# Kernel tuning notes

Hardware: AMD Instinct MI355X
Metric: run time of the kernel (lower is better)

The kernel has to match this reference:

```python
import jax, jax.numpy as jnp
import numpy as np

B, C, CI, T, H, W = 4, 256, 128, 8, 28, 28
EPS = 1e-5


def setup_inputs() -> dict:
    key = jax.random.key(0)
    ks = jax.random.split(key, 12)
    s = 0.02
    return {
        "x": jax.random.normal(ks[0], (B, C, T, H, W), jnp.float32),
        "Wg": jax.random.normal(ks[1], (CI, C), jnp.float32) * s,
        "bg": jax.random.normal(ks[2], (CI,), jnp.float32) * s,
        "Wt": jax.random.normal(ks[3], (CI, C), jnp.float32) * s,
        "bt": jax.random.normal(ks[4], (CI,), jnp.float32) * s,
        "Wp": jax.random.normal(ks[5], (CI, C), jnp.float32) * s,
        "bp": jax.random.normal(ks[6], (CI,), jnp.float32) * s,
        "Ww": jax.random.normal(ks[7], (C, CI), jnp.float32) * s,
        "bw": jax.random.normal(ks[8], (C,), jnp.float32) * s,
        "gamma": jax.random.normal(ks[9], (C,), jnp.float32) * s + 1.0,
        "beta": jax.random.normal(ks[10], (C,), jnp.float32) * s,
        "rmean": jax.random.normal(ks[11], (C,), jnp.float32) * s,
        "rvar": jax.random.uniform(jax.random.fold_in(key, 99), (C,), jnp.float32, 0.5, 1.5),
    }


def reference(x, Wg, bg, Wt, bt, Wp, bp, Ww, bw, gamma, beta, rmean, rvar):
    b, c, t, h, w = x.shape
    n = t * h * w
    xf = x.reshape(b, c, n)                                   # [B,C,N]
    # 1x1x1 conv projections == per-position linear maps
    g = jnp.einsum('oc,bcn->bno', Wg, xf) + bg                # [B,N,Ci]
    th = jnp.einsum('oc,bcn->bno', Wt, xf) + bt               # [B,N,Ci]
    ph = jnp.einsum('oc,bcn->bon', Wp, xf) + bp[None, :, None]  # [B,Ci,N]
    f = jnp.einsum('bnc,bcm->bnm', th, ph)                    # [B,N,N] attention logits
    attn = jax.nn.softmax(f, axis=-1)
    y = jnp.einsum('bnm,bmo->bno', attn, g)                   # [B,N,Ci]
    wy = jnp.einsum('co,bno->bcn', Ww, y) + bw[None, :, None]  # [B,C,N]
    # BatchNorm3d (eval mode: running stats)
    inv = gamma / jnp.sqrt(rvar + EPS)
    wy = wy * inv[None, :, None] + (beta - rmean * inv)[None, :, None]
    z = wy + xf                                               # residual
    return z.reshape(b, c, t, h, w)
```

## Files before the change

kernel.cpp:

```cpp
#include <hip/hip_runtime.h>
#include <hip/hip_bf16.h>
#include <hip/hip_fp8.h>

#define BB 4
#define CC 256
#define CI 128
#define NN 6272
#define LOG2E 1.4426950408889634f

#define KSTRIDE 136
#define VSTRIDE 72
#define KBUF (64 * KSTRIDE)
#define VBUF (128 * VSTRIDE)

typedef __attribute__((ext_vector_type(8))) __bf16 bf16x8;
typedef __attribute__((ext_vector_type(4))) __bf16 bf16x4;
typedef __attribute__((ext_vector_type(4))) float f32x4;
typedef __attribute__((ext_vector_type(16))) float f32x16;

__device__ __forceinline__ unsigned cvtpk_fp8(float a, float b) {
  unsigned r;
  asm("v_cvt_pk_fp8_f32 %0, %1, %2" : "=v"(r) : "v"(a), "v"(b));
  return r;
}

__device__ __forceinline__ unsigned char to_fp8(float v) {
  __hip_fp8_e4m3 t(v);
  return *reinterpret_cast<unsigned char*>(&t);
}

__global__ void nlb_prep(const float* __restrict__ Wg, const float* __restrict__ bg,
                         const float* __restrict__ Wt, const float* __restrict__ bt,
                         const float* __restrict__ Wp, const float* __restrict__ bp,
                         const float* __restrict__ Ww, const float* __restrict__ bw,
                         const float* __restrict__ gamma, const float* __restrict__ beta,
                         const float* __restrict__ rmean, const float* __restrict__ rvar,
                         __bf16* __restrict__ wall, float* __restrict__ ball,
                         __bf16* __restrict__ wwb, float* __restrict__ scale,
                         float* __restrict__ shift) {
  int idx = blockIdx.x * 256 + threadIdx.x;
  if (idx < 384 * 256) {
    int o = idx >> 8, c = idx & 255;
    float v, bv;
    if (o < 128)      { v = Wt[o * 256 + c] * LOG2E;  bv = bt[o] * LOG2E; }
    else if (o < 256) { v = Wp[(o - 128) * 256 + c]; bv = bp[o - 128]; }
    else              { v = Wg[(o - 256) * 256 + c]; bv = bg[o - 256]; }
    wall[idx] = (__bf16)v;
    if (c == 0) ball[o] = bv;
  } else if (idx < 384 * 256 + 256 * 128) {
    int i = idx - 384 * 256;
    wwb[i] = (__bf16)Ww[i];
  } else if (idx < 384 * 256 + 256 * 128 + 256) {
    int c = idx - (384 * 256 + 256 * 128);
    float inv = gamma[c] * rsqrtf(rvar[c] + 1e-5f);
    scale[c] = inv;
    shift[c] = (bw[c] - rmean[c]) * inv + beta[c];
  }
}

__launch_bounds__(256)
__global__ void nlb_proj(const float* __restrict__ x, const __bf16* __restrict__ wall,
                         const float* __restrict__ ball,
                         unsigned char* __restrict__ Q8, unsigned char* __restrict__ K8,
                         unsigned char* __restrict__ V8t) {
  const int nb = blockIdx.x;
  const int b  = blockIdx.y;
  const int tid = threadIdx.x;
  const int lane = tid & 63, w = tid >> 6;
  const int n0 = nb * 64;
  const int r = lane & 15, g = lane >> 4;

  __shared__ __bf16 xl[64][40];

  const float* xb = x + (size_t)b * CC * NN;
  f32x4 acc[6][4] = {};

  const int snn = tid & 63;
  const int skg = tid >> 6;

  for (int k0 = 0; k0 < 256; k0 += 32) {
    bf16x8 tmp;
#pragma unroll
    for (int i = 0; i < 8; ++i)
      tmp[i] = (__bf16)xb[(size_t)(k0 + skg * 8 + i) * NN + n0 + snn];
    __syncthreads();
    *reinterpret_cast<bf16x8*>(&xl[snn][skg * 8]) = tmp;
    __syncthreads();

    bf16x8 bfrag[4];
#pragma unroll
    for (int j = 0; j < 4; ++j)
      bfrag[j] = *reinterpret_cast<const bf16x8*>(&xl[j * 16 + r][g * 8]);
#pragma unroll
    for (int mb = 0; mb < 6; ++mb) {
      bf16x8 afrag = *reinterpret_cast<const bf16x8*>(
          &wall[(size_t)(mb * 64 + w * 16 + r) * 256 + k0 + g * 8]);
#pragma unroll
      for (int j = 0; j < 4; ++j)
        acc[mb][j] = __builtin_amdgcn_mfma_f32_16x16x32_bf16(afrag, bfrag[j], acc[mb][j], 0, 0, 0);
    }
  }

#pragma unroll
  for (int mb = 0; mb < 6; ++mb) {
    const int m0 = mb * 64 + w * 16;
    if (m0 < 256) {
      unsigned char* dst = (m0 < 128) ? Q8 : K8;
      const int obase = (m0 < 128) ? m0 : (m0 - 128);
#pragma unroll
      for (int j = 0; j < 4; ++j) {
        int n = n0 + j * 16 + r;
        union { unsigned char bch[4]; unsigned u; } pk;
#pragma unroll
        for (int reg = 0; reg < 4; ++reg) {
          int o = m0 + g * 4 + reg;
          pk.bch[reg] = to_fp8(acc[mb][j][reg] + ball[o]);
        }
        *reinterpret_cast<unsigned*>(&dst[((size_t)b * NN + n) * CI + obase + g * 4]) = pk.u;
      }
    } else {
#pragma unroll
      for (int j = 0; j < 4; ++j) {
        int n = n0 + j * 16 + r;
#pragma unroll
        for (int reg = 0; reg < 4; ++reg) {
          int o = m0 + g * 4 + reg;
          float v = acc[mb][j][reg] + ball[o];
          V8t[((size_t)b * CI + (o - 256)) * NN + n] = to_fp8(v);
        }
      }
    }
  }
}

__launch_bounds__(256, 2)
__global__ void nlb_attn(const unsigned char* __restrict__ Q8,
                         const unsigned char* __restrict__ K8,
                         const unsigned char* __restrict__ V8t,
                         __bf16* __restrict__ Y) {
  const int bid = blockIdx.x;
  const int swz = (bid & 7) * 49 + (bid >> 3);
  const int b  = swz / 98;
  const int qb = swz % 98;
  const int tid = threadIdx.x, lane = tid & 63, w = tid >> 6;
  const int c = lane & 31, hi = lane >> 5;
  const int wq = w & 1, h = w >> 1;
  const int q0 = qb * 64 + wq * 32;

  const unsigned char* Qb = Q8  + (size_t)b * NN * CI;
  const char* Kb = (const char*)(K8 + (size_t)b * NN * CI);
  const char* Vb = (const char*)(V8t + (size_t)b * CI * NN);

  __shared__ __align__(16) char sm[2 * KBUF + 2 * VBUF];
  __shared__ float mls[2][64];

  uint4 gk0, gk1, gv0, gv1;
  const char* ksrc = Kb + tid * 32;
  const char* vsrc = Vb + (size_t)(tid >> 1) * NN + (tid & 1) * 32;
  auto gload = [&]() {
    gk0 = *reinterpret_cast<const uint4*>(ksrc);
    gk1 = *reinterpret_cast<const uint4*>(ksrc + 16);
    gv0 = *reinterpret_cast<const uint4*>(vsrc);
    gv1 = *reinterpret_cast<const uint4*>(vsrc + 16);
    ksrc += 8192; vsrc += 64;
  };
  char* const kd_base = sm + (tid >> 2) * KSTRIDE + (tid & 3) * 32;
  char* const vd_base = sm + 2 * KBUF + (tid >> 1) * VSTRIDE + (tid & 1) * 32;
  auto swrite = [&](int bb) {
    char* kd = kd_base + bb * KBUF;
    *reinterpret_cast<uint2*>(kd + 0)  = make_uint2(gk0.x, gk0.y);
    *reinterpret_cast<uint2*>(kd + 8)  = make_uint2(gk0.z, gk0.w);
    *reinterpret_cast<uint2*>(kd + 16) = make_uint2(gk1.x, gk1.y);
    *reinterpret_cast<uint2*>(kd + 24) = make_uint2(gk1.z, gk1.w);
    char* vd = vd_base + bb * VBUF;
    *reinterpret_cast<uint2*>(vd + 0)  = make_uint2(gv0.x, gv0.y);
    *reinterpret_cast<uint2*>(vd + 8)  = make_uint2(gv0.z, gv0.w);
    *reinterpret_cast<uint2*>(vd + 16) = make_uint2(gv1.x, gv1.y);
    *reinterpret_cast<uint2*>(vd + 24) = make_uint2(gv1.z, gv1.w);
  };

  long qf[8];
#pragma unroll
  for (int kc = 0; kc < 8; ++kc)
    qf[kc] = *reinterpret_cast<const long*>(&Qb[(size_t)(q0 + c) * CI + kc * 16 + hi * 8]);

  f32x16 yacc[4] = {};
  float l_acc = 0.f;

  gload();
  swrite(0);
  __syncthreads();

  int buf = 0;
  for (int t = 0; t < 98; ++t) {
    if (t + 1 < 98) gload();
    const char* kl = sm + buf * KBUF;
    const char* vl = sm + 2 * KBUF + buf * VBUF;

    f32x16 s;
#pragma unroll
    for (int i = 0; i < 16; ++i) s[i] = -4.f;
    __builtin_amdgcn_s_setprio(1);
#pragma unroll
    for (int kc = 0; kc < 8; ++kc) {
      long kf = *reinterpret_cast<const long*>(
          kl + (h * 32 + c) * KSTRIDE + kc * 16 + hi * 8);
      s = __builtin_amdgcn_mfma_f32_32x32x16_fp8_fp8(kf, qf[kc], s, 0, 0, 0);
    }
    __builtin_amdgcn_s_setprio(0);

#pragma unroll
    for (int reg = 0; reg < 16; ++reg) s[reg] = exp2f(s[reg]);
    float l0 = ((s[0] + s[1]) + (s[2] + s[3])) + ((s[4] + s[5]) + (s[6] + s[7]));
    float l1 = ((s[8] + s[9]) + (s[10] + s[11])) + ((s[12] + s[13]) + (s[14] + s[15]));
    l_acc += l0 + l1;

    unsigned pw[4];
#pragma unroll
    for (int i = 0; i < 4; ++i) {
      unsigned lo  = cvtpk_fp8(s[4 * i + 0], s[4 * i + 1]);
      unsigned hi2 = cvtpk_fp8(s[4 * i + 2], s[4 * i + 3]);
      pw[i] = __builtin_amdgcn_perm(hi2, lo, 0x05040100);
    }

    __builtin_amdgcn_s_setprio(1);
#pragma unroll
    for (int ch = 0; ch < 2; ++ch) {
      unsigned A = pw[ch * 2 + 0], B = pw[ch * 2 + 1];
      unsigned sX = (unsigned)__shfl_xor((int)(hi ? A : B), 32);
      unsigned plo = hi ? sX : A;
      unsigned phi = hi ? B : sX;
      long pa = (long)(((unsigned long long)phi << 32) | plo);
#pragma unroll
      for (int cb = 0; cb < 4; ++cb) {
        long vf = *reinterpret_cast<const long*>(
            vl + (cb * 32 + c) * VSTRIDE + h * 32 + ch * 16 + hi * 8);
        yacc[cb] = __builtin_amdgcn_mfma_f32_32x32x16_fp8_fp8(pa, vf, yacc[cb], 0, 0, 0);
      }
    }
    __builtin_amdgcn_s_setprio(0);

    if (t + 1 < 98) swrite(buf ^ 1);
    __syncthreads();
    buf ^= 1;
  }

  float l_full = l_acc + __shfl_xor(l_acc, 32);

  float* scr = (float*)sm;
  if (h == 1) {
    float* base = scr + wq * 4096;
#pragma unroll
    for (int cb = 0; cb < 4; ++cb)
#pragma unroll
      for (int reg = 0; reg < 16; ++reg)
        base[(cb * 16 + reg) * 64 + lane] = yacc[cb][reg];
    mls[wq][lane] = l_full;
  }
  __syncthreads();
  if (h == 0) {
    const float* base = scr + wq * 4096;
    float il = 1.f / (l_full + mls[wq][lane]);
    float ilq[16];
#pragma unroll
    for (int reg = 0; reg < 16; ++reg) {
      int qloc = (reg & 3) + 8 * (reg >> 2) + 4 * hi;
      ilq[reg] = __shfl(il, qloc);
    }
#pragma unroll
    for (int cb = 0; cb < 4; ++cb) {
#pragma unroll
      for (int reg = 0; reg < 16; ++reg) {
        int qloc = (reg & 3) + 8 * (reg >> 2) + 4 * hi;
        float v = (yacc[cb][reg] + base[(cb * 16 + reg) * 64 + lane]) * ilq[reg];
        Y[((size_t)b * NN + q0 + qloc) * CI + cb * 32 + c] = (__bf16)v;
      }
    }
  }
}

__launch_bounds__(256)
__global__ void nlb_out(const __bf16* __restrict__ Y, const __bf16* __restrict__ wwb,
                        const float* __restrict__ scale, const float* __restrict__ shift,
                        const float* __restrict__ x, float* __restrict__ out) {
  const int nb = blockIdx.x;
  const int mb = blockIdx.y;
  const int b  = blockIdx.z;
  const int tid = threadIdx.x, lane = tid & 63, w = tid >> 6;
  const int r = lane & 15, g = lane >> 4;
  const int n0 = nb * 64, c0 = mb * 64 + w * 16;

  const __bf16* Yb = Y + (size_t)b * NN * CI;
  f32x4 acc[4] = {};
#pragma unroll
  for (int k0 = 0; k0 < 128; k0 += 32) {
    bf16x8 af = *reinterpret_cast<const bf16x8*>(&wwb[(size_t)(c0 + r) * CI + k0 + g * 8]);
#pragma unroll
    for (int j = 0; j < 4; ++j) {
      bf16x8 bfg = *reinterpret_cast<const bf16x8*>(
          &Yb[(size_t)(n0 + j * 16 + r) * CI + k0 + g * 8]);
      acc[j] = __builtin_amdgcn_mfma_f32_16x16x32_bf16(af, bfg, acc[j], 0, 0, 0);
    }
  }
  const float* xb = x + (size_t)b * CC * NN;
  float* ob = out + (size_t)b * CC * NN;
#pragma unroll
  for (int j = 0; j < 4; ++j) {
    int n = n0 + j * 16 + r;
#pragma unroll
    for (int reg = 0; reg < 4; ++reg) {
      int cc = c0 + g * 4 + reg;
      size_t off = (size_t)cc * NN + n;
      ob[off] = acc[j][reg] * scale[cc] + shift[cc] + xb[off];
    }
  }
}

extern "C" void kernel_launch(void* const* d_in, const int* in_sizes, int n_in,
                              void* d_out, int out_size, void* d_ws, size_t ws_size,
                              hipStream_t stream) {
  (void)in_sizes; (void)n_in; (void)out_size; (void)ws_size;
  const float* x     = (const float*)d_in[0];
  const float* Wg    = (const float*)d_in[1];
  const float* bg    = (const float*)d_in[2];
  const float* Wt    = (const float*)d_in[3];
  const float* bt    = (const float*)d_in[4];
  const float* Wp    = (const float*)d_in[5];
  const float* bp    = (const float*)d_in[6];
  const float* Ww    = (const float*)d_in[7];
  const float* bw    = (const float*)d_in[8];
  const float* gamma = (const float*)d_in[9];
  const float* beta  = (const float*)d_in[10];
  const float* rmean = (const float*)d_in[11];
  const float* rvar  = (const float*)d_in[12];
  float* out = (float*)d_out;

  char* ws = (char*)d_ws;
  __bf16* wall = (__bf16*)(ws + 0);
  float*  ball = (float*)(ws + 196608);
  __bf16* wwb  = (__bf16*)(ws + 198144);
  float*  scl  = (float*)(ws + 263680);
  float*  shf  = (float*)(ws + 264704);
  unsigned char* Q8 = (unsigned char*)(ws + 265728);
  unsigned char* K8 = (unsigned char*)(ws + 3476992);
  unsigned char* V8 = (unsigned char*)(ws + 6688256);
  __bf16* Yw   = (__bf16*)(ws + 9899520);

  nlb_prep<<<513, 256, 0, stream>>>(Wg, bg, Wt, bt, Wp, bp, Ww, bw, gamma, beta,
                                    rmean, rvar, wall, ball, wwb, scl, shf);
  nlb_proj<<<dim3(98, 4), 256, 0, stream>>>(x, wall, ball, Q8, K8, V8);
  nlb_attn<<<392, 256, 0, stream>>>(Q8, K8, V8, Yw);
  nlb_out<<<dim3(98, 4, 4), 256, 0, stream>>>(Yw, wwb, scl, shf, x, out);
}
```

Before: 171.2 us.

## Split attention keys across two blocks and merge partials in output GEMM

```diff
diff --git a/kernel.cpp b/kernel.cpp
--- a/kernel.cpp
+++ b/kernel.cpp
@@ -133,19 +133,20 @@
   }
 }
 
-__launch_bounds__(256, 2)
+__launch_bounds__(256, 4)
 __global__ void nlb_attn(const unsigned char* __restrict__ Q8,
                          const unsigned char* __restrict__ K8,
                          const unsigned char* __restrict__ V8t,
-                         __bf16* __restrict__ Y) {
+                         __bf16* __restrict__ Yp, float* __restrict__ Lp) {
   const int bid = blockIdx.x;
-  const int swz = (bid & 7) * 49 + (bid >> 3);
-  const int b  = swz / 98;
-  const int qb = swz % 98;
+  const int pair = bid & 7;
+  const int b  = pair >> 1, ks = pair & 1;
+  const int qb = bid >> 3;
   const int tid = threadIdx.x, lane = tid & 63, w = tid >> 6;
   const int c = lane & 31, hi = lane >> 5;
   const int wq = w & 1, h = w >> 1;
   const int q0 = qb * 64 + wq * 32;
+  const int NT = 49;
 
   const unsigned char* Qb = Q8  + (size_t)b * NN * CI;
   const char* Kb = (const char*)(K8 + (size_t)b * NN * CI);
@@ -155,8 +156,8 @@
   __shared__ float mls[2][64];
 
   uint4 gk0, gk1, gv0, gv1;
-  const char* ksrc = Kb + tid * 32;
-  const char* vsrc = Vb + (size_t)(tid >> 1) * NN + (tid & 1) * 32;
+  const char* ksrc = Kb + (size_t)(ks * NT) * 8192 + tid * 32;
+  const char* vsrc = Vb + (size_t)(tid >> 1) * NN + (ks * NT) * 64 + (tid & 1) * 32;
   auto gload = [&]() {
     gk0 = *reinterpret_cast<const uint4*>(ksrc);
     gk1 = *reinterpret_cast<const uint4*>(ksrc + 16);
@@ -192,8 +193,8 @@
   __syncthreads();
 
   int buf = 0;
-  for (int t = 0; t < 98; ++t) {
-    if (t + 1 < 98) gload();
+  for (int t = 0; t < NT; ++t) {
+    if (t + 1 < NT) gload();
     const char* kl = sm + buf * KBUF;
     const char* vl = sm + 2 * KBUF + buf * VBUF;
 
@@ -240,7 +241,7 @@
     }
     __builtin_amdgcn_s_setprio(0);
 
-    if (t + 1 < 98) swrite(buf ^ 1);
+    if (t + 1 < NT) swrite(buf ^ 1);
     __syncthreads();
     buf ^= 1;
   }
@@ -260,27 +261,25 @@
   __syncthreads();
   if (h == 0) {
     const float* base = scr + wq * 4096;
-    float il = 1.f / (l_full + mls[wq][lane]);
-    float ilq[16];
-#pragma unroll
-    for (int reg = 0; reg < 16; ++reg) {
-      int qloc = (reg & 3) + 8 * (reg >> 2) + 4 * hi;
-      ilq[reg] = __shfl(il, qloc);
-    }
+    float lsum = l_full + mls[wq][lane];
+    if (hi == 0)
+      Lp[(size_t)(ks * 4 + b) * NN + q0 + c] = lsum;
+    __bf16* Yb = Yp + (size_t)(ks * 4 + b) * NN * CI;
 #pragma unroll
     for (int cb = 0; cb < 4; ++cb) {
 #pragma unroll
       for (int reg = 0; reg < 16; ++reg) {
         int qloc = (reg & 3) + 8 * (reg >> 2) + 4 * hi;
-        float v = (yacc[cb][reg] + base[(cb * 16 + reg) * 64 + lane]) * ilq[reg];
-        Y[((size_t)b * NN + q0 + qloc) * CI + cb * 32 + c] = (__bf16)v;
+        float v = yacc[cb][reg] + base[(cb * 16 + reg) * 64 + lane];
+        Yb[(size_t)(q0 + qloc) * CI + cb * 32 + c] = (__bf16)v;
       }
     }
   }
 }
 
 __launch_bounds__(256)
-__global__ void nlb_out(const __bf16* __restrict__ Y, const __bf16* __restrict__ wwb,
+__global__ void nlb_out(const __bf16* __restrict__ Yp, const float* __restrict__ Lp,
+                        const __bf16* __restrict__ wwb,
                         const float* __restrict__ scale, const float* __restrict__ shift,
                         const float* __restrict__ x, float* __restrict__ out) {
   const int nb = blockIdx.x;
@@ -290,16 +289,19 @@
   const int r = lane & 15, g = lane >> 4;
   const int n0 = nb * 64, c0 = mb * 64 + w * 16;
 
-  const __bf16* Yb = Y + (size_t)b * NN * CI;
+  const __bf16* Y0 = Yp + (size_t)b * NN * CI;
+  const __bf16* Y1 = Yp + (size_t)(4 + b) * NN * CI;
   f32x4 acc[4] = {};
 #pragma unroll
   for (int k0 = 0; k0 < 128; k0 += 32) {
     bf16x8 af = *reinterpret_cast<const bf16x8*>(&wwb[(size_t)(c0 + r) * CI + k0 + g * 8]);
 #pragma unroll
     for (int j = 0; j < 4; ++j) {
-      bf16x8 bfg = *reinterpret_cast<const bf16x8*>(
-          &Yb[(size_t)(n0 + j * 16 + r) * CI + k0 + g * 8]);
-      acc[j] = __builtin_amdgcn_mfma_f32_16x16x32_bf16(af, bfg, acc[j], 0, 0, 0);
+      size_t yoff = (size_t)(n0 + j * 16 + r) * CI + k0 + g * 8;
+      bf16x8 bf0 = *reinterpret_cast<const bf16x8*>(&Y0[yoff]);
+      acc[j] = __builtin_amdgcn_mfma_f32_16x16x32_bf16(af, bf0, acc[j], 0, 0, 0);
+      bf16x8 bf1 = *reinterpret_cast<const bf16x8*>(&Y1[yoff]);
+      acc[j] = __builtin_amdgcn_mfma_f32_16x16x32_bf16(af, bf1, acc[j], 0, 0, 0);
     }
   }
   const float* xb = x + (size_t)b * CC * NN;
@@ -307,11 +309,12 @@
 #pragma unroll
   for (int j = 0; j < 4; ++j) {
     int n = n0 + j * 16 + r;
+    float il = 1.f / (Lp[(size_t)b * NN + n] + Lp[(size_t)(4 + b) * NN + n]);
 #pragma unroll
     for (int reg = 0; reg < 4; ++reg) {
       int cc = c0 + g * 4 + reg;
       size_t off = (size_t)cc * NN + n;
-      ob[off] = acc[j][reg] * scale[cc] + shift[cc] + xb[off];
+      ob[off] = acc[j][reg] * (il * scale[cc]) + shift[cc] + xb[off];
     }
   }
 }
@@ -344,11 +347,12 @@
   unsigned char* Q8 = (unsigned char*)(ws + 265728);
   unsigned char* K8 = (unsigned char*)(ws + 3476992);
   unsigned char* V8 = (unsigned char*)(ws + 6688256);
-  __bf16* Yw   = (__bf16*)(ws + 9899520);
+  __bf16* Yp   = (__bf16*)(ws + 9899520);
+  float*  Lp   = (float*)(ws + 22744576);
 
   nlb_prep<<<513, 256, 0, stream>>>(Wg, bg, Wt, bt, Wp, bp, Ww, bw, gamma, beta,
                                     rmean, rvar, wall, ball, wwb, scl, shf);
   nlb_proj<<<dim3(98, 4), 256, 0, stream>>>(x, wall, ball, Q8, K8, V8);
-  nlb_attn<<<392, 256, 0, stream>>>(Q8, K8, V8, Yw);
-  nlb_out<<<dim3(98, 4, 4), 256, 0, stream>>>(Yw, wwb, scl, shf, x, out);
-}
+  nlb_attn<<<784, 256, 0, stream>>>(Q8, K8, V8, Yp, Lp);
+  nlb_out<<<dim3(98, 4, 4), 256, 0, stream>>>(Yp, Lp, wwb, scl, shf, x, out);
+}
```

Result: slower. 195.7 us (+14.3%).

## Give each wave private K/V LDS buffers and drop per-tile block barriers

Applied to the files above, without the earlier changes.

```diff
diff --git a/kernel.cpp b/kernel.cpp
--- a/kernel.cpp
+++ b/kernel.cpp
@@ -9,9 +9,10 @@
 #define LOG2E 1.4426950408889634f
 
 #define KSTRIDE 136
-#define VSTRIDE 72
-#define KBUF (64 * KSTRIDE)
-#define VBUF (128 * VSTRIDE)
+#define VSTRIDE 40
+#define KWBUF (32 * KSTRIDE)
+#define VWBUF (128 * VSTRIDE)
+#define WBUF (KWBUF + VWBUF)
 
 typedef __attribute__((ext_vector_type(8))) __bf16 bf16x8;
 typedef __attribute__((ext_vector_type(4))) __bf16 bf16x4;
@@ -151,32 +152,40 @@
   const char* Kb = (const char*)(K8 + (size_t)b * NN * CI);
   const char* Vb = (const char*)(V8t + (size_t)b * CI * NN);
 
-  __shared__ __align__(16) char sm[2 * KBUF + 2 * VBUF];
+  __shared__ __align__(16) char sm[4 * 2 * WBUF];
   __shared__ float mls[2][64];
 
-  uint4 gk0, gk1, gv0, gv1;
-  const char* ksrc = Kb + tid * 32;
-  const char* vsrc = Vb + (size_t)(tid >> 1) * NN + (tid & 1) * 32;
-  auto gload = [&]() {
-    gk0 = *reinterpret_cast<const uint4*>(ksrc);
-    gk1 = *reinterpret_cast<const uint4*>(ksrc + 16);
-    gv0 = *reinterpret_cast<const uint4*>(vsrc);
-    gv1 = *reinterpret_cast<const uint4*>(vsrc + 16);
-    ksrc += 8192; vsrc += 64;
+  char* const wbase = sm + w * (2 * WBUF);
+
+  const char* const ksrc = Kb + (size_t)(h * 32) * CI + lane * 16;
+  const char* const vsrc = Vb + (size_t)(lane >> 1) * NN + h * 32 + (lane & 1) * 16;
+
+  uint4 gk[4], gv[4];
+  auto gload = [&](int t) {
+    const char* kp = ksrc + (size_t)t * 8192;
+#pragma unroll
+    for (int i = 0; i < 4; ++i)
+      gk[i] = *reinterpret_cast<const uint4*>(kp + i * 1024);
+    const char* vp = vsrc + t * 64;
+#pragma unroll
+    for (int i = 0; i < 4; ++i)
+      gv[i] = *reinterpret_cast<const uint4*>(vp + (size_t)i * 32 * NN);
   };
-  char* const kd_base = sm + (tid >> 2) * KSTRIDE + (tid & 3) * 32;
-  char* const vd_base = sm + 2 * KBUF + (tid >> 1) * VSTRIDE + (tid & 1) * 32;
   auto swrite = [&](int bb) {
-    char* kd = kd_base + bb * KBUF;
-    *reinterpret_cast<uint2*>(kd + 0)  = make_uint2(gk0.x, gk0.y);
-    *reinterpret_cast<uint2*>(kd + 8)  = make_uint2(gk0.z, gk0.w);
-    *reinterpret_cast<uint2*>(kd + 16) = make_uint2(gk1.x, gk1.y);
-    *reinterpret_cast<uint2*>(kd + 24) = make_uint2(gk1.z, gk1.w);
-    char* vd = vd_base + bb * VBUF;
-    *reinterpret_cast<uint2*>(vd + 0)  = make_uint2(gv0.x, gv0.y);
-    *reinterpret_cast<uint2*>(vd + 8)  = make_uint2(gv0.z, gv0.w);
-    *reinterpret_cast<uint2*>(vd + 16) = make_uint2(gv1.x, gv1.y);
-    *reinterpret_cast<uint2*>(vd + 24) = make_uint2(gv1.z, gv1.w);
+    char* base = wbase + bb * WBUF;
+#pragma unroll
+    for (int i = 0; i < 4; ++i) {
+      char* kd = base + (i * 8 + (lane >> 3)) * KSTRIDE + (lane & 7) * 16;
+      *reinterpret_cast<uint2*>(kd + 0) = make_uint2(gk[i].x, gk[i].y);
+      *reinterpret_cast<uint2*>(kd + 8) = make_uint2(gk[i].z, gk[i].w);
+    }
+    char* vb2 = base + KWBUF;
+#pragma unroll
+    for (int i = 0; i < 4; ++i) {
+      char* vd = vb2 + (i * 32 + (lane >> 1)) * VSTRIDE + (lane & 1) * 16;
+      *reinterpret_cast<uint2*>(vd + 0) = make_uint2(gv[i].x, gv[i].y);
+      *reinterpret_cast<uint2*>(vd + 8) = make_uint2(gv[i].z, gv[i].w);
+    }
   };
 
   long qf[8];
@@ -187,15 +196,13 @@
   f32x16 yacc[4] = {};
   float l_acc = 0.f;
 
-  gload();
+  gload(0);
   swrite(0);
-  __syncthreads();
-
-  int buf = 0;
+
   for (int t = 0; t < 98; ++t) {
-    if (t + 1 < 98) gload();
-    const char* kl = sm + buf * KBUF;
-    const char* vl = sm + 2 * KBUF + buf * VBUF;
+    if (t < 97) gload(t + 1);
+    const char* kl = wbase + (t & 1) * WBUF;
+    const char* vl = kl + KWBUF;
 
     f32x16 s;
 #pragma unroll
@@ -203,8 +210,7 @@
     __builtin_amdgcn_s_setprio(1);
 #pragma unroll
     for (int kc = 0; kc < 8; ++kc) {
-      long kf = *reinterpret_cast<const long*>(
-          kl + (h * 32 + c) * KSTRIDE + kc * 16 + hi * 8);
+      long kf = *reinterpret_cast<const long*>(kl + c * KSTRIDE + kc * 16 + hi * 8);
       s = __builtin_amdgcn_mfma_f32_32x32x16_fp8_fp8(kf, qf[kc], s, 0, 0, 0);
     }
     __builtin_amdgcn_s_setprio(0);
@@ -222,6 +228,8 @@
       unsigned hi2 = cvtpk_fp8(s[4 * i + 2], s[4 * i + 3]);
       pw[i] = __builtin_amdgcn_perm(hi2, lo, 0x05040100);
     }
+
+    if (t < 97) swrite((t + 1) & 1);
 
     __builtin_amdgcn_s_setprio(1);
 #pragma unroll
@@ -234,20 +242,17 @@
 #pragma unroll
       for (int cb = 0; cb < 4; ++cb) {
         long vf = *reinterpret_cast<const long*>(
-            vl + (cb * 32 + c) * VSTRIDE + h * 32 + ch * 16 + hi * 8);
+            vl + (cb * 32 + c) * VSTRIDE + ch * 16 + hi * 8);
         yacc[cb] = __builtin_amdgcn_mfma_f32_32x32x16_fp8_fp8(pa, vf, yacc[cb], 0, 0, 0);
       }
     }
     __builtin_amdgcn_s_setprio(0);
-
-    if (t + 1 < 98) swrite(buf ^ 1);
-    __syncthreads();
-    buf ^= 1;
   }
 
   float l_full = l_acc + __shfl_xor(l_acc, 32);
 
   float* scr = (float*)sm;
+  __syncthreads();
   if (h == 1) {
     float* base = scr + wq * 4096;
 #pragma unroll
```

Result: no change. 171.6 us (+0.3%).
